# Kernel optimization log

Measured on AMD Instinct MI355X. Metric: run time of the kernel, lower is better.

Reference implementation:

```python
import jax, jax.numpy as jnp
import numpy as np

EMBED, IN_DIM, HID, LAYERS, NVIEW = 1024, 256, 256, 3, 6


def _lstm_layer(x_seq, Wih, Whh, bih, bhh):
    # x_seq: [BM, N, D]; torch LSTM gate order i,f,g,o
    BM = x_seq.shape[0]
    h0 = jnp.zeros((BM, HID), x_seq.dtype)
    c0 = jnp.zeros((BM, HID), x_seq.dtype)

    def step(carry, x_t):
        h, c = carry
        gates = x_t @ Wih.T + bih + h @ Whh.T + bhh  # [BM, 4H]
        i, f, g, o = jnp.split(gates, 4, axis=-1)
        c = jax.nn.sigmoid(f) * c + jax.nn.sigmoid(i) * jnp.tanh(g)
        h = jax.nn.sigmoid(o) * jnp.tanh(c)
        return (h, c), h

    _, ys = jax.lax.scan(step, (h0, c0), jnp.swapaxes(x_seq, 0, 1))
    return jnp.swapaxes(ys, 0, 1)  # [BM, N, H]


def setup_inputs() -> dict:
    key = jax.random.key(0)
    ks = jax.random.split(key, 16)
    B, M = 32, 256
    s = lambda fan: 1.0 / np.sqrt(fan)
    inp = {
        "b_x_swin": jax.random.normal(ks[0], (B, M, NVIEW, EMBED), jnp.float32),
        "b_x_conv": jax.random.normal(ks[1], (B, M, NVIEW, EMBED), jnp.float32),
        "Wc": jax.random.uniform(ks[2], (EMBED, EMBED), jnp.float32, -s(EMBED), s(EMBED)),
        "bc": jax.random.uniform(ks[3], (EMBED,), jnp.float32, -s(EMBED), s(EMBED)),
        "Win": jax.random.uniform(ks[4], (IN_DIM, EMBED), jnp.float32, -s(EMBED), s(EMBED)),
        "b_in": jax.random.uniform(ks[5], (IN_DIM,), jnp.float32, -s(EMBED), s(EMBED)),
        "Wih": jax.random.uniform(ks[6], (LAYERS, 4 * HID, IN_DIM), jnp.float32, -s(HID), s(HID)),
        "Whh": jax.random.uniform(ks[7], (LAYERS, 4 * HID, HID), jnp.float32, -s(HID), s(HID)),
        "bih": jax.random.uniform(ks[8], (LAYERS, 4 * HID), jnp.float32, -s(HID), s(HID)),
        "bhh": jax.random.uniform(ks[9], (LAYERS, 4 * HID), jnp.float32, -s(HID), s(HID)),
        "Wv": jax.random.uniform(ks[10], (1, HID), jnp.float32, -s(HID), s(HID)),
        "bv": jax.random.uniform(ks[11], (1,), jnp.float32, -s(HID), s(HID)),
        "Ws": jax.random.uniform(ks[12], (1, NVIEW), jnp.float32, -s(NVIEW), s(NVIEW)),
        "bs": jax.random.uniform(ks[13], (1,), jnp.float32, -s(NVIEW), s(NVIEW)),
    }
    return inp


def reference(b_x_swin, b_x_conv, Wc, bc, Win, b_in, Wih, Whh, bih, bhh, Wv, bv, Ws, bs):
    B, M, N, C = b_x_swin.shape
    # fc_conv + exact GELU + residual (vectorized over all samples; same math as per-sample loop)
    x = b_x_swin + jax.nn.gelu(b_x_conv @ Wc.T + bc, approximate=False)
    x = x @ Win.T + b_in                         # [B, M, N, IN_DIM]
    x = x.reshape(B * M, N, IN_DIM)              # LSTM batch = B*M, seq = N
    for l in range(LAYERS):
        x = _lstm_layer(x, Wih[l], Whh[l], bih[l], bhh[l])
    v = (x @ Wv.T + bv).reshape(B, M, N)         # fc_viewport + flatten(1)
    score = (v @ Ws.T + bs).squeeze(-1)          # fc_score -> [B, M]
    return jnp.mean(score, axis=1)               # torch.mean per sample -> [B]
```

## Files before the change

### kernel.cpp

```cpp
#include <hip/hip_runtime.h>
#include <math.h>
#include <stdint.h>

typedef unsigned short u16;
typedef float f32x4 __attribute__((ext_vector_type(4)));
typedef short bf16x8 __attribute__((ext_vector_type(8)));

#define NVIEW 6

__device__ __forceinline__ u16 f2bf(float f){
  unsigned u = __float_as_uint(f);
  u += 0x7FFFu + ((u >> 16) & 1u);
  return (u16)(u >> 16);
}
__device__ __forceinline__ float bf2f(u16 h){
  return __uint_as_float(((unsigned)h) << 16);
}
__device__ __forceinline__ float fsig(float x){
  x = fminf(fmaxf(x, -30.f), 30.f);
  return 1.0f / (1.0f + __expf(-x));
}
__device__ __forceinline__ float ftanh(float x){
  x = fminf(fmaxf(x, -15.f), 15.f);
  float e = __expf(2.0f * x);
  return (e - 1.0f) / (e + 1.0f);
}
__device__ __forceinline__ float gelu_exact(float v){
  float x  = v * 0.70710678118654752f;
  float ax = fabsf(x);
  float t  = 1.0f / fmaf(0.3275911f, ax, 1.0f);
  float p  = t * fmaf(t, fmaf(t, fmaf(t, fmaf(t, 1.061405429f, -1.453152027f),
                                      1.421413741f), -0.284496736f), 0.254829592f);
  float er = copysignf(1.0f - p * __expf(-ax * ax), x);
  return 0.5f * v * (1.0f + er);
}
__device__ __forceinline__ void gload16(const u16* g, u16* l){
  __builtin_amdgcn_global_load_lds((const __attribute__((address_space(1))) unsigned int*)g,
                                   (__attribute__((address_space(3))) unsigned int*)l,
                                   16, 0, 0);
}

__global__ void k_cvt(const float* __restrict__ in, u16* __restrict__ out, long n4){
  long i = (long)blockIdx.x * blockDim.x + threadIdx.x;
  long stride = (long)gridDim.x * blockDim.x;
  for (; i < n4; i += stride){
    const float4 v = ((const float4*)in)[i];
    ushort4 o;
    o.x = f2bf(v.x); o.y = f2bf(v.y); o.z = f2bf(v.z); o.w = f2bf(v.w);
    ((ushort4*)out)[i] = o;
  }
}

__global__ void k_build_wl(const float* __restrict__ Wih, const float* __restrict__ Whh,
                           u16* __restrict__ Wl){
  int idx = blockIdx.x * 256 + threadIdx.x;
  int l   = idx >> 19;
  int rem = idx & 524287;
  int ro  = rem >> 9;
  int k   = rem & 511;
  int u = ro >> 2, q = ro & 3;
  int ri = q * 256 + u;
  float v = (k < 256) ? Wih[(l * 1024 + ri) * 256 + k]
                      : Whh[(l * 1024 + ri) * 256 + (k - 256)];
  Wl[idx] = f2bf(v);
}

__global__ void k_build_bias(const float* __restrict__ bih, const float* __restrict__ bhh,
                             float* __restrict__ biasL, u16* __restrict__ zbuf){
  int idx = blockIdx.x * 256 + threadIdx.x;
  if (idx < 3072){
    int l = idx >> 10; int ro = idx & 1023;
    int u = ro >> 2, q = ro & 3;
    int ri = q * 256 + u;
    biasL[idx] = bih[l * 1024 + ri] + bhh[l * 1024 + ri];
  }
  if (idx < 256) zbuf[idx] = 0;
}

template<int EPI>
__global__ __launch_bounds__(256, 2)
void gemm_dr(const u16* __restrict__ A0, long sA0,
             const u16* __restrict__ A1, long sA1, int K0,
             const u16* __restrict__ Bm, long sB,
             int N, int K, int NBn,
             const float* __restrict__ bias,
             const float* __restrict__ resid,
             u16* __restrict__ outb,
             float* __restrict__ cbuf,
             int tstep)
{
  __shared__ __align__(16) u16 lA[5 * 4096];
  __shared__ __align__(16) u16 lB[5 * 4096];

  const int tid  = threadIdx.x;
  const int lane = tid & 63;
  const int wid  = tid >> 6;
  const int wm = wid >> 1, wn = wid & 1;
  const int l15 = lane & 15, lk = lane >> 4;

  const int nwg = gridDim.x;
  const int qx  = nwg >> 3;
  const int bb  = blockIdx.x;
  const int swz = (bb & 7) * qx + (bb >> 3);
  const long m0 = (long)(swz / NBn) * 128;
  const int  n0 = (swz % NBn) * 128;
  const int  NT = K >> 5;

  const int rA0 = tid >> 2;
  const int cA  = tid & 3;
  const int slog = (((rA0 & 1) << 2) | cA) ^ ((rA0 >> 1) & 7);
  const int srow = (rA0 & ~1) | (slog >> 2);
  const int scol = (slog & 3) << 3;
  const int ldst = rA0 * 32 + cA * 8;

  auto STAGE = [&](int slot, int t){
    const int kb = t << 5;
    const int so = slot * 4096;
    #pragma unroll
    for (int c = 0; c < 2; ++c){
      const int r  = c * 64 + srow;
      const int gc = kb + scol;
      const u16* s = (gc < K0) ? (A0 + (m0 + r) * sA0 + gc)
                               : (A1 + (m0 + r) * sA1 + (gc - K0));
      gload16(s, &lA[so + c * 2048 + ldst]);
    }
    #pragma unroll
    for (int c = 0; c < 2; ++c){
      const int r  = c * 64 + srow;
      const int gc = kb + scol;
      gload16(Bm + (long)(n0 + r) * sB + gc, &lB[so + c * 2048 + ldst]);
    }
  };

  f32x4 acc[4][4];
  #pragma unroll
  for (int i = 0; i < 4; ++i)
    #pragma unroll
    for (int j = 0; j < 4; ++j)
      acc[i][j] = (f32x4){0.f, 0.f, 0.f, 0.f};

  const int spA = (((l15 & 1) << 2) | lk) ^ (l15 >> 1);
  const int rdA = (wm * 32 + (l15 >> 1)) * 64 + spA * 8;
  const int rdB = (wn * 32 + (l15 >> 1)) * 64 + spA * 8;

  auto COMPUTE = [&](int slot){
    const int so = slot * 4096;
    bf16x8 af[4], bq[4];
    #pragma unroll
    for (int mf = 0; mf < 4; ++mf)
      af[mf] = *(const bf16x8*)&lA[so + rdA + mf * 512];
    #pragma unroll
    for (int nf = 0; nf < 4; ++nf)
      bq[nf] = *(const bf16x8*)&lB[so + rdB + nf * 512];
    #pragma unroll
    for (int mf = 0; mf < 4; ++mf)
      #pragma unroll
      for (int nf = 0; nf < 4; ++nf)
        acc[mf][nf] = __builtin_amdgcn_mfma_f32_16x16x32_bf16(af[mf], bq[nf], acc[mf][nf], 0, 0, 0);
  };

  STAGE(0, 0); STAGE(1, 1); STAGE(2, 2); STAGE(3, 3);

  int sr = 0, sw = 4;
  for (int t = 0; t + 4 <= NT; ++t){
    asm volatile("s_waitcnt vmcnt(12)" ::: "memory");
    asm volatile("s_barrier" ::: "memory");
    if (t + 4 < NT){ STAGE(sw, t + 4); }
    COMPUTE(sr);
    sr = (sr == 4) ? 0 : sr + 1;
    sw = (sw == 4) ? 0 : sw + 1;
  }
  asm volatile("s_waitcnt vmcnt(8)" ::: "memory");
  asm volatile("s_barrier" ::: "memory");
  COMPUTE(sr); sr = (sr == 4) ? 0 : sr + 1;
  asm volatile("s_waitcnt vmcnt(4)" ::: "memory");
  asm volatile("s_barrier" ::: "memory");
  COMPUTE(sr); sr = (sr == 4) ? 0 : sr + 1;
  asm volatile("s_waitcnt vmcnt(0)" ::: "memory");
  asm volatile("s_barrier" ::: "memory");
  COMPUTE(sr);

  if (EPI == 0 || EPI == 1){
    #pragma unroll
    for (int mf = 0; mf < 4; ++mf){
      #pragma unroll
      for (int nf = 0; nf < 4; ++nf){
        int  n    = n0 + wn * 64 + nf * 16 + l15;
        long mrow = m0 + wm * 64 + mf * 16 + lk * 4;
        float bz = bias[n];
        #pragma unroll
        for (int r = 0; r < 4; ++r){
          float v = acc[mf][nf][r] + bz;
          long off = (mrow + r) * N + n;
          if (EPI == 0) v = gelu_exact(v) + resid[off];
          outb[off] = f2bf(v);
        }
      }
    }
  } else {
    const int a  = lane & 3;
    const int qb = lane & ~3;
    #pragma unroll
    for (int mf = 0; mf < 4; ++mf){
      #pragma unroll
      for (int nf = 0; nf < 4; ++nf){
        int n = n0 + wn * 64 + nf * 16 + l15;
        float bz = bias[n];
        float v0 = acc[mf][nf][0] + bz;
        float v1 = acc[mf][nf][1] + bz;
        float v2 = acc[mf][nf][2] + bz;
        float v3 = acc[mf][nf][3] + bz;
        float s0 = (a == 0) ? v0 : (a == 1) ? v1 : (a == 2) ? v2 : v3;
        float s1 = (a == 0) ? v1 : (a == 1) ? v2 : (a == 2) ? v3 : v0;
        float s2 = (a == 0) ? v2 : (a == 1) ? v3 : (a == 2) ? v0 : v1;
        float s3 = (a == 0) ? v3 : (a == 1) ? v0 : (a == 2) ? v1 : v2;
        float r0 = s0;
        float r1 = __shfl(s1, qb + ((a + 3) & 3));
        float r2 = __shfl(s2, qb + ((a + 2) & 3));
        float r3 = __shfl(s3, qb + ((a + 1) & 3));
        float wi = (a == 0) ? r0 : (a == 1) ? r1 : (a == 2) ? r2 : r3;
        float wf = (a == 1) ? r0 : (a == 2) ? r1 : (a == 3) ? r2 : r3;
        float wg = (a == 2) ? r0 : (a == 3) ? r1 : (a == 0) ? r2 : r3;
        float wo = (a == 3) ? r0 : (a == 0) ? r1 : (a == 1) ? r2 : r3;
        long row = m0 + wm * 64 + mf * 16 + lk * 4 + a;
        int  u   = ((n0 + wn * 64 + nf * 16) >> 2) + (l15 >> 2);
        float c_old = (tstep == 0) ? 0.0f : cbuf[row * 256 + u];
        float ii = fsig(wi), ff = fsig(wf), gg = ftanh(wg), oo = fsig(wo);
        float cn = ff * c_old + ii * gg;
        float hn = oo * ftanh(cn);
        cbuf[row * 256 + u] = cn;
        outb[(row * NVIEW + tstep) * 256 + u] = f2bf(hn);
      }
    }
  }
}

__global__ void k_score(const u16* __restrict__ X3, const float* __restrict__ Wv,
                        const float* __restrict__ bv, const float* __restrict__ Ws,
                        const float* __restrict__ bs, float* __restrict__ score){
  int lane = threadIdx.x & 63;
  int bm = blockIdx.x * 4 + (threadIdx.x >> 6);
  const u16* row = X3 + (long)bm * (NVIEW * 256);
  float4 wv = *(const float4*)(Wv + lane * 4);
  float p = 0.f;
  #pragma unroll
  for (int n = 0; n < NVIEW; ++n){
    ushort4 xv = *(const ushort4*)(row + n * 256 + lane * 4);
    float d = bf2f(xv.x) * wv.x + bf2f(xv.y) * wv.y + bf2f(xv.z) * wv.z + bf2f(xv.w) * wv.w;
    p += Ws[n] * d;
  }
  #pragma unroll
  for (int off = 32; off; off >>= 1) p += __shfl_xor(p, off);
  if (lane == 0){
    float sw = Ws[0] + Ws[1] + Ws[2] + Ws[3] + Ws[4] + Ws[5];
    score[bm] = p + bv[0] * sw + bs[0];
  }
}

__global__ void k_mean(const float* __restrict__ score, float* __restrict__ out){
  __shared__ float red[256];
  int b = blockIdx.x, tid = threadIdx.x;
  red[tid] = score[b * 256 + tid];
  __syncthreads();
  for (int s = 128; s > 0; s >>= 1){
    if (tid < s) red[tid] += red[tid + s];
    __syncthreads();
  }
  if (tid == 0) out[b] = red[0] * (1.0f / 256.0f);
}

extern "C" void kernel_launch(void* const* d_in, const int* in_sizes, int n_in,
                              void* d_out, int out_size, void* d_ws, size_t ws_size,
                              hipStream_t stream){
  const float* swin = (const float*)d_in[0];
  const float* conv = (const float*)d_in[1];
  const float* Wc   = (const float*)d_in[2];
  const float* bc   = (const float*)d_in[3];
  const float* Win  = (const float*)d_in[4];
  const float* b_in = (const float*)d_in[5];
  const float* Wih  = (const float*)d_in[6];
  const float* Whh  = (const float*)d_in[7];
  const float* bih  = (const float*)d_in[8];
  const float* bhh  = (const float*)d_in[9];
  const float* Wv   = (const float*)d_in[10];
  const float* bv   = (const float*)d_in[11];
  const float* Ws   = (const float*)d_in[12];
  const float* bs   = (const float*)d_in[13];
  float* out = (float*)d_out;

  char* w = (char*)d_ws;
  u16*  convb = (u16*)(w);
  u16*  X0    = (u16*)(w);
  u16*  XA    = (u16*)(w + 25165824);
  u16*  XB    = (u16*)(w + 50331648);
  float* cbuf = (float*)(w + 75497472);
  u16*  Y     = (u16*)(w + 100663296);
  u16*  Wcb   = (u16*)(w + 201326592);
  u16*  Winb  = (u16*)(w + 203423744);
  u16*  Wl    = (u16*)(w + 203948032);
  float* biasL= (float*)(w + 207093760);
  u16*  zbuf  = (u16*)(w + 207106048);
  float* scoreb = (float*)(w + 207106560);

  k_cvt<<<4096, 256, 0, stream>>>(conv, convb, 49152L * 1024 / 4);
  k_cvt<<<512, 256, 0, stream>>>(Wc, Wcb, 1048576 / 4);
  k_cvt<<<128, 256, 0, stream>>>(Win, Winb, 262144 / 4);
  k_build_wl<<<6144, 256, 0, stream>>>(Wih, Whh, Wl);
  k_build_bias<<<12, 256, 0, stream>>>(bih, bhh, biasL, zbuf);

  gemm_dr<0><<<3072, 256, 0, stream>>>(
      convb, 1024L, convb, 1024L, 1024,
      Wcb, 1024L, 1024, 1024, 8, bc, swin, Y, (float*)nullptr, 0);

  gemm_dr<1><<<768, 256, 0, stream>>>(
      Y, 1024L, Y, 1024L, 1024,
      Winb, 1024L, 256, 1024, 2, b_in, (const float*)nullptr, X0, (float*)nullptr, 0);

  const u16* xin = X0;
  u16* xout = XA;
  for (int l = 0; l < 3; ++l){
    for (int t = 0; t < 6; ++t){
      const u16* a1 = (t == 0) ? zbuf : (xout + (t - 1) * 256);
      long s1 = (t == 0) ? 0L : 1536L;
      gemm_dr<2><<<512, 256, 0, stream>>>(
          xin + t * 256, 1536L, a1, s1, 256,
          Wl + l * 1024 * 512, 512L, 1024, 512, 8,
          biasL + l * 1024, (const float*)nullptr,
          xout, cbuf, t);
    }
    if (l == 0){ xin = XA; xout = XB; }
    else if (l == 1){ xin = XB; xout = XA; }
  }

  k_score<<<2048, 256, 0, stream>>>(XA, Wv, bv, Ws, bs, scoreb);
  k_mean<<<32, 256, 0, stream>>>(scoreb, out);
}
```

Before: 739.1 us.

## Replace fc_conv GEMM with 256x256-tile 8-wave ping-pong pipelined kernel

Adds a new gemm8 kernel that computes the large fc_conv GEMM (49152x1024x1024) with 256x256 output tiles over 512-thread blocks. It uses double-buffered swizzled LDS, inline ds_read_b128 with immediate offsets, explicit waitcnt and barrier phasing, and setprio around the MFMA bursts. The larger tile is meant to raise data reuse per block and overlap global loads with MFMA work, cutting memory traffic and LDS stalls. In exchange it uses 128KB of LDS, heavy register pressure and hand-scheduled synchronization. It also assumes K is a multiple of 128.

```diff
diff --git a/kernel.cpp b/kernel.cpp
--- a/kernel.cpp
+++ b/kernel.cpp
@@ -75,6 +75,141 @@
     biasL[idx] = bih[l * 1024 + ri] + bhh[l * 1024 + ri];
   }
   if (idx < 256) zbuf[idx] = 0;
+}
+
+#define DSRI(dst, addr, imm) \
+  asm volatile("ds_read_b128 %0, %1 offset:%2" : "=v"(dst) : "v"(addr), "i"(imm))
+
+template<int EPI>
+__global__ __launch_bounds__(512, 2)
+void gemm8(const u16* __restrict__ A, long sA,
+           const u16* __restrict__ Bm, long sB,
+           int N, int K, int NBn,
+           const float* __restrict__ bias,
+           const float* __restrict__ resid,
+           u16* __restrict__ outb)
+{
+  __shared__ __align__(128) u16 sh[65536];
+
+  const int tid  = threadIdx.x;
+  const int lane = tid & 63;
+  const int wv   = tid >> 6;
+  const int wm   = wv >> 2;
+  const int wn   = wv & 3;
+  const int l15  = lane & 15, lk = lane >> 4;
+  const int w2   = wv * 2;
+
+  const int nwg = gridDim.x;
+  const int qx  = nwg >> 3;
+  const int bb  = blockIdx.x;
+  const int swz = (bb & 7) * qx + (bb >> 3);
+  const long m0 = (long)(swz / NBn) * 256;
+  const int  n0 = (swz % NBn) * 256;
+  const int  NT  = K >> 6;
+  const int  NIT = NT >> 1;
+
+  const u16* aSrc = A  + (m0 + (lane >> 3)) * sA + (((lane & 7) ^ (lane >> 3)) << 3);
+  const u16* bSrc = Bm + ((long)n0 + (lane >> 3)) * sB + (((lane & 7) ^ (lane >> 3)) << 3);
+
+  auto STA8 = [&](int buf, int half, int t){
+    const u16* s = aSrc + ((long)(half * 128 + w2 * 8)) * sA + ((long)t << 6);
+    u16* d = &sh[buf * 16384 + half * 8192 + w2 * 512 + lane * 8];
+    gload16(s, d);
+    gload16(s + 8 * sA, d + 512);
+  };
+  auto STB8 = [&](int buf, int half, int t){
+    const u16* s = bSrc + ((long)(half * 128 + w2 * 8)) * sB + ((long)t << 6);
+    u16* d = &sh[32768 + buf * 16384 + half * 8192 + w2 * 512 + lane * 8];
+    gload16(s, d);
+    gload16(s + 8 * sB, d + 512);
+  };
+
+  const unsigned ldsBase = (unsigned)(uintptr_t)&sh[0];
+  const unsigned spb = (unsigned)((lk ^ (l15 & 7)) << 4);
+  const unsigned aRd0 = ldsBase + wm * 16384 + l15 * 128 + spb;
+  const unsigned aRd1 = aRd0 ^ 64;
+  const unsigned bRd0 = ldsBase + 65536 + (wn >> 1) * 16384 + ((wn & 1) * 64 + l15) * 128 + spb;
+  const unsigned bRd1 = bRd0 ^ 64;
+
+#define RDA(BUF, G, KS, DST) do{ const unsigned _a = (KS) ? aRd1 : aRd0;          \
+    DSRI(DST[0], _a, (BUF)*32768 + (G)*8192 + 0);                                 \
+    DSRI(DST[1], _a, (BUF)*32768 + (G)*8192 + 2048);                              \
+    DSRI(DST[2], _a, (BUF)*32768 + (G)*8192 + 4096);                              \
+    DSRI(DST[3], _a, (BUF)*32768 + (G)*8192 + 6144); }while(0)
+#define RDB(BUF, KS, DST) do{ const unsigned _b = (KS) ? bRd1 : bRd0;             \
+    DSRI(DST[0], _b, (BUF)*32768 + 0);                                            \
+    DSRI(DST[1], _b, (BUF)*32768 + 2048);                                         \
+    DSRI(DST[2], _b, (BUF)*32768 + 4096);                                         \
+    DSRI(DST[3], _b, (BUF)*32768 + 6144); }while(0)
+
+  f32x4 acc[8][4];
+  #pragma unroll
+  for (int i = 0; i < 8; ++i)
+    #pragma unroll
+    for (int j = 0; j < 4; ++j)
+      acc[i][j] = (f32x4){0.f, 0.f, 0.f, 0.f};
+
+  bf16x8 aF0[4], aF1[4], bF0[4], bF1[4];
+
+  STA8(0, 0, 0); STA8(0, 1, 0); STB8(0, 0, 0); STB8(0, 1, 0);
+  STB8(1, 0, 1); STB8(1, 1, 1);
+  asm volatile("s_waitcnt vmcnt(4)" ::: "memory");
+  __builtin_amdgcn_s_barrier();
+  RDA(0, 0, 0, aF0); RDB(0, 0, bF0);
+
+#define PH(G, AU, BU, RDS, STG, VM) {                                             \
+    RDS;                                                                          \
+    STG;                                                                          \
+    __builtin_amdgcn_s_barrier();                                                 \
+    asm volatile("s_waitcnt lgkmcnt(0)" ::: "memory");                            \
+    __builtin_amdgcn_sched_barrier(0);                                            \
+    __builtin_amdgcn_s_setprio(1);                                                \
+    _Pragma("unroll") for (int i = 0; i < 4; ++i)                                 \
+      _Pragma("unroll") for (int nf = 0; nf < 4; ++nf)                            \
+        acc[(G)*4 + i][nf] = __builtin_amdgcn_mfma_f32_16x16x32_bf16(             \
+            AU[i], BU[nf], acc[(G)*4 + i][nf], 0, 0, 0);                          \
+    __builtin_amdgcn_s_setprio(0);                                                \
+    VM;                                                                           \
+    __builtin_amdgcn_s_barrier(); }
+
+#define VM2C { if (nl) { asm volatile("s_waitcnt vmcnt(2)" ::: "memory"); }        \
+               else    { asm volatile("s_waitcnt vmcnt(0)" ::: "memory"); } }
+#define NOVM { }
+
+  for (int I = 0; I < NIT; ++I){
+    const int t1 = 2 * I + 1;
+    const bool nl = (I < NIT - 1);
+    PH(0, aF0, bF0, RDA(0,1,0,aF1),                 STA8(1,0,t1),               NOVM)
+    PH(1, aF1, bF0, { RDA(0,0,1,aF0); RDB(0,1,bF1);}, STA8(1,1,t1),             NOVM)
+    PH(0, aF0, bF1, RDA(0,1,1,aF1),                 if (nl) STB8(0,0,t1+1);,    VM2C)
+    PH(1, aF1, bF1, { RDA(1,0,0,aF0); RDB(1,0,bF0);}, if (nl) STB8(0,1,t1+1);, NOVM)
+    PH(0, aF0, bF0, RDA(1,1,0,aF1),                 if (nl) STA8(0,0,t1+1);,    NOVM)
+    PH(1, aF1, bF0, { RDA(1,0,1,aF0); RDB(1,1,bF1);}, if (nl) STA8(0,1,t1+1);, NOVM)
+    PH(0, aF0, bF1, RDA(1,1,1,aF1),                 if (nl) STB8(1,0,t1+2);,    VM2C)
+    PH(1, aF1, bF1, { RDA(0,0,0,aF0); RDB(0,0,bF0);}, if (nl) STB8(1,1,t1+2);, NOVM)
+  }
+#undef PH
+#undef VM2C
+#undef NOVM
+#undef RDA
+#undef RDB
+
+  #pragma unroll
+  for (int mf = 0; mf < 8; ++mf){
+    #pragma unroll
+    for (int nf = 0; nf < 4; ++nf){
+      const int n = n0 + wn * 64 + nf * 16 + l15;
+      const float bz = bias[n];
+      const long mrow = m0 + wm * 128 + mf * 16 + lk * 4;
+      #pragma unroll
+      for (int r = 0; r < 4; ++r){
+        float v = acc[mf][nf][r] + bz;
+        const long off = (mrow + r) * (long)N + n;
+        if (EPI == 0) v = gelu_exact(v) + resid[off];
+        outb[off] = f2bf(v);
+      }
+    }
+  }
 }
 
 template<int EPI>
@@ -308,9 +443,8 @@
   k_build_wl<<<6144, 256, 0, stream>>>(Wih, Whh, Wl);
   k_build_bias<<<12, 256, 0, stream>>>(bih, bhh, biasL, zbuf);
 
-  gemm_dr<0><<<3072, 256, 0, stream>>>(
-      convb, 1024L, convb, 1024L, 1024,
-      Wcb, 1024L, 1024, 1024, 8, bc, swin, Y, (float*)nullptr, 0);
+  gemm8<0><<<768, 512, 0, stream>>>(convb, 1024L, Wcb, 1024L,
+                                    1024, 1024, 4, bc, swin, Y);
 
   gemm_dr<1><<<768, 256, 0, stream>>>(
       Y, 1024L, Y, 1024L, 1024,
```

After: 812.7 us. 1.1x slower.

## Fuse all LSTM layers and timesteps into one persistent kernel

Applied to the files above, without the earlier changes.

Replaces the 18 per-timestep GEMM launches with a single k_lstm kernel. Each block owns 32 sequences across all 3 layers and 6 steps, keeping the cell state in registers and h in LDS, and streams the weights through a 3-slot LDS ring. This removes the launch overhead, the cbuf global round trips and the re-reading of h from global memory. In exchange only 256 blocks at occupancy 1 run, and every block re-streams the full weight set from L2 at each step.

```diff
diff --git a/kernel.cpp b/kernel.cpp
--- a/kernel.cpp
+++ b/kernel.cpp
@@ -66,7 +66,7 @@
 }
 
 __global__ void k_build_bias(const float* __restrict__ bih, const float* __restrict__ bhh,
-                             float* __restrict__ biasL, u16* __restrict__ zbuf){
+                             float* __restrict__ biasL){
   int idx = blockIdx.x * 256 + threadIdx.x;
   if (idx < 3072){
     int l = idx >> 10; int ro = idx & 1023;
@@ -74,20 +74,16 @@
     int ri = q * 256 + u;
     biasL[idx] = bih[l * 1024 + ri] + bhh[l * 1024 + ri];
   }
-  if (idx < 256) zbuf[idx] = 0;
 }
 
 template<int EPI>
 __global__ __launch_bounds__(256, 2)
 void gemm_dr(const u16* __restrict__ A0, long sA0,
-             const u16* __restrict__ A1, long sA1, int K0,
              const u16* __restrict__ Bm, long sB,
              int N, int K, int NBn,
              const float* __restrict__ bias,
              const float* __restrict__ resid,
-             u16* __restrict__ outb,
-             float* __restrict__ cbuf,
-             int tstep)
+             u16* __restrict__ outb)
 {
   __shared__ __align__(16) u16 lA[5 * 4096];
   __shared__ __align__(16) u16 lB[5 * 4096];
@@ -119,16 +115,12 @@
     #pragma unroll
     for (int c = 0; c < 2; ++c){
       const int r  = c * 64 + srow;
-      const int gc = kb + scol;
-      const u16* s = (gc < K0) ? (A0 + (m0 + r) * sA0 + gc)
-                               : (A1 + (m0 + r) * sA1 + (gc - K0));
-      gload16(s, &lA[so + c * 2048 + ldst]);
+      gload16(A0 + (m0 + r) * sA0 + (kb + scol), &lA[so + c * 2048 + ldst]);
     }
     #pragma unroll
     for (int c = 0; c < 2; ++c){
       const int r  = c * 64 + srow;
-      const int gc = kb + scol;
-      gload16(Bm + (long)(n0 + r) * sB + gc, &lB[so + c * 2048 + ldst]);
+      gload16(Bm + (long)(n0 + r) * sB + (kb + scol), &lB[so + c * 2048 + ldst]);
     }
   };
 
@@ -180,56 +172,170 @@
   asm volatile("s_barrier" ::: "memory");
   COMPUTE(sr);
 
-  if (EPI == 0 || EPI == 1){
-    #pragma unroll
-    for (int mf = 0; mf < 4; ++mf){
-      #pragma unroll
-      for (int nf = 0; nf < 4; ++nf){
-        int  n    = n0 + wn * 64 + nf * 16 + l15;
-        long mrow = m0 + wm * 64 + mf * 16 + lk * 4;
-        float bz = bias[n];
+  #pragma unroll
+  for (int mf = 0; mf < 4; ++mf){
+    #pragma unroll
+    for (int nf = 0; nf < 4; ++nf){
+      int  n    = n0 + wn * 64 + nf * 16 + l15;
+      long mrow = m0 + wm * 64 + mf * 16 + lk * 4;
+      float bz = bias[n];
+      #pragma unroll
+      for (int r = 0; r < 4; ++r){
+        float v = acc[mf][nf][r] + bz;
+        long off = (mrow + r) * N + n;
+        if (EPI == 0) v = gelu_exact(v) + resid[off];
+        outb[off] = f2bf(v);
+      }
+    }
+  }
+}
+
+__global__ __launch_bounds__(256, 1)
+void k_lstm(const u16* __restrict__ X0, const u16* __restrict__ Wl,
+            const float* __restrict__ biasL,
+            u16* __restrict__ HA, u16* __restrict__ HB)
+{
+  __shared__ __align__(16) u16 lA[16384];
+  __shared__ __align__(16) u16 lB[3 * 16384];
+
+  const int tid  = threadIdx.x;
+  const int lane = tid & 63;
+  const int wv   = tid >> 6;
+  const int l15  = lane & 15, lk = lane >> 4;
+  const int ax   = l15 & 7;
+  const int spB  = (((l15 & 1) << 2) | lk) ^ (l15 >> 1);
+  const int a    = lane & 3;
+  const int qb   = lane & ~3;
+  const long R   = (long)blockIdx.x * 32;
+
+  const int rB0 = tid >> 2;
+  const int cB  = tid & 3;
+  const int slogB = (((rB0 & 1) << 2) | cB) ^ ((rB0 >> 1) & 7);
+  const int srowB = (rB0 & ~1) | (slogB >> 2);
+  const int scolB = (slogB & 3) << 3;
+  const int ldstB = rB0 * 32 + cB * 8;
+
+  auto STB = [&](int g){
+    if (g < 576){
+      const int lw  = g / 192;
+      const int hcl = g % 32;
+      const int ring = g % 3;
+      const u16* src = Wl + (long)lw * 524288 + (long)(hcl & 1) * 262144 + (hcl >> 1) * 32;
+      u16* dst = &lB[ring * 16384];
+      #pragma unroll
+      for (int ch = 0; ch < 8; ++ch)
+        gload16(src + (long)(ch * 64 + srowB) * 512 + scolB, dst + ch * 2048 + ldstB);
+    }
+  };
+
+  const int xr_ = tid >> 3;
+  const int xcb = tid & 7;
+  const int xk  = xr_ & 7;
+
+  f32x4 acc[2][2][8];
+  float cc[2][2][8];
+  float bv[2][8];
+
+  int g = 0;
+  STB(0); STB(1);
+
+  for (int l = 0; l < 3; ++l){
+    const u16* xsrc = (l == 0) ? X0 : ((l == 1) ? HA : HB);
+    u16* hdst = (l == 1) ? HB : HA;
+    #pragma unroll
+    for (int hf = 0; hf < 2; ++hf)
+      #pragma unroll
+      for (int nt = 0; nt < 8; ++nt){
+        bv[hf][nt] = biasL[l * 1024 + hf * 512 + wv * 128 + nt * 16 + l15];
         #pragma unroll
-        for (int r = 0; r < 4; ++r){
-          float v = acc[mf][nf][r] + bz;
-          long off = (mrow + r) * N + n;
-          if (EPI == 0) v = gelu_exact(v) + resid[off];
-          outb[off] = f2bf(v);
-        }
+        for (int mt = 0; mt < 2; ++mt) cc[mt][hf][nt] = 0.f;
       }
-    }
-  } else {
-    const int a  = lane & 3;
-    const int qb = lane & ~3;
-    #pragma unroll
-    for (int mf = 0; mf < 4; ++mf){
-      #pragma unroll
-      for (int nf = 0; nf < 4; ++nf){
-        int n = n0 + wn * 64 + nf * 16 + l15;
-        float bz = bias[n];
-        float v0 = acc[mf][nf][0] + bz;
-        float v1 = acc[mf][nf][1] + bz;
-        float v2 = acc[mf][nf][2] + bz;
-        float v3 = acc[mf][nf][3] + bz;
-        float s0 = (a == 0) ? v0 : (a == 1) ? v1 : (a == 2) ? v2 : v3;
-        float s1 = (a == 0) ? v1 : (a == 1) ? v2 : (a == 2) ? v3 : v0;
-        float s2 = (a == 0) ? v2 : (a == 1) ? v3 : (a == 2) ? v0 : v1;
-        float s3 = (a == 0) ? v3 : (a == 1) ? v0 : (a == 2) ? v1 : v2;
-        float r0 = s0;
-        float r1 = __shfl(s1, qb + ((a + 3) & 3));
-        float r2 = __shfl(s2, qb + ((a + 2) & 3));
-        float r3 = __shfl(s3, qb + ((a + 1) & 3));
-        float wi = (a == 0) ? r0 : (a == 1) ? r1 : (a == 2) ? r2 : r3;
-        float wf = (a == 1) ? r0 : (a == 2) ? r1 : (a == 3) ? r2 : r3;
-        float wg = (a == 2) ? r0 : (a == 3) ? r1 : (a == 0) ? r2 : r3;
-        float wo = (a == 3) ? r0 : (a == 0) ? r1 : (a == 1) ? r2 : r3;
-        long row = m0 + wm * 64 + mf * 16 + lk * 4 + a;
-        int  u   = ((n0 + wn * 64 + nf * 16) >> 2) + (l15 >> 2);
-        float c_old = (tstep == 0) ? 0.0f : cbuf[row * 256 + u];
-        float ii = fsig(wi), ff = fsig(wf), gg = ftanh(wg), oo = fsig(wo);
-        float cn = ff * c_old + ii * gg;
-        float hn = oo * ftanh(cn);
-        cbuf[row * 256 + u] = cn;
-        outb[(row * NVIEW + tstep) * 256 + u] = f2bf(hn);
+    __syncthreads();
+    {
+      bf16x8 z = (bf16x8){0,0,0,0,0,0,0,0};
+      #pragma unroll
+      for (int j = 0; j < 4; ++j)
+        *(bf16x8*)&lA[xr_ * 512 + (32 + ((4 * xcb + j) ^ xk)) * 8] = z;
+    }
+    for (int t = 0; t < 6; ++t){
+      bf16x8 xv[4];
+      const u16* xp = xsrc + ((R + xr_) * 6 + t) * 256 + xcb * 32;
+      #pragma unroll
+      for (int j = 0; j < 4; ++j) xv[j] = *(const bf16x8*)(xp + j * 8);
+      __syncthreads();
+      #pragma unroll
+      for (int mt = 0; mt < 2; ++mt)
+        #pragma unroll
+        for (int hf = 0; hf < 2; ++hf)
+          #pragma unroll
+          for (int nt = 0; nt < 8; ++nt)
+            acc[mt][hf][nt] = (f32x4){0.f, 0.f, 0.f, 0.f};
+      #pragma unroll
+      for (int j = 0; j < 4; ++j)
+        *(bf16x8*)&lA[xr_ * 512 + ((4 * xcb + j) ^ xk) * 8] = xv[j];
+      asm volatile("s_waitcnt lgkmcnt(0)" ::: "memory");
+      __builtin_amdgcn_s_barrier();
+
+#define HALF(HF)                                                               \
+      {                                                                        \
+        asm volatile("s_waitcnt vmcnt(8)" ::: "memory");                       \
+        asm volatile("s_barrier" ::: "memory");                                \
+        STB(g + 2);                                                            \
+        const int ring = g % 3;                                                \
+        bf16x8 af[2], bq[8];                                                   \
+        _Pragma("unroll") for (int mt = 0; mt < 2; ++mt)                       \
+          af[mt] = *(const bf16x8*)&lA[(mt * 16 + l15) * 512 +                 \
+                                       ((ktc * 4 + lk) ^ ax) * 8];             \
+        _Pragma("unroll") for (int nt = 0; nt < 8; ++nt)                       \
+          bq[nt] = *(const bf16x8*)&lB[ring * 16384 +                          \
+                     (wv * 64 + nt * 8 + (l15 >> 1)) * 64 + spB * 8];          \
+        _Pragma("unroll") for (int mt = 0; mt < 2; ++mt)                       \
+          _Pragma("unroll") for (int nt = 0; nt < 8; ++nt)                     \
+            acc[mt][HF][nt] = __builtin_amdgcn_mfma_f32_16x16x32_bf16(         \
+                af[mt], bq[nt], acc[mt][HF][nt], 0, 0, 0);                     \
+        ++g;                                                                   \
+      }
+      for (int ktc = 0; ktc < 16; ++ktc){ HALF(0) HALF(1) }
+#undef HALF
+
+      #pragma unroll
+      for (int mt = 0; mt < 2; ++mt)
+        #pragma unroll
+        for (int hf = 0; hf < 2; ++hf)
+          #pragma unroll
+          for (int nt = 0; nt < 8; ++nt){
+            const float bz = bv[hf][nt];
+            float v0 = acc[mt][hf][nt][0] + bz;
+            float v1 = acc[mt][hf][nt][1] + bz;
+            float v2 = acc[mt][hf][nt][2] + bz;
+            float v3 = acc[mt][hf][nt][3] + bz;
+            float s0 = (a == 0) ? v0 : (a == 1) ? v1 : (a == 2) ? v2 : v3;
+            float s1 = (a == 0) ? v1 : (a == 1) ? v2 : (a == 2) ? v3 : v0;
+            float s2 = (a == 0) ? v2 : (a == 1) ? v3 : (a == 2) ? v0 : v1;
+            float s3 = (a == 0) ? v3 : (a == 1) ? v0 : (a == 2) ? v1 : v2;
+            float r0 = s0;
+            float r1 = __shfl(s1, qb + ((a + 3) & 3));
+            float r2 = __shfl(s2, qb + ((a + 2) & 3));
+            float r3 = __shfl(s3, qb + ((a + 1) & 3));
+            float wi = (a == 0) ? r0 : (a == 1) ? r1 : (a == 2) ? r2 : r3;
+            float wf = (a == 1) ? r0 : (a == 2) ? r1 : (a == 3) ? r2 : r3;
+            float wg = (a == 2) ? r0 : (a == 3) ? r1 : (a == 0) ? r2 : r3;
+            float wo = (a == 3) ? r0 : (a == 0) ? r1 : (a == 1) ? r2 : r3;
+            const int rloc = mt * 16 + lk * 4 + a;
+            const int u    = hf * 128 + wv * 32 + nt * 4 + (l15 >> 2);
+            float co = cc[mt][hf][nt];
+            float ii = fsig(wi), ff = fsig(wf), gg = ftanh(wg), oo = fsig(wo);
+            float cn = ff * co + ii * gg;
+            float hn = oo * ftanh(cn);
+            cc[mt][hf][nt] = cn;
+            lA[rloc * 512 + (32 + ((u >> 3) ^ (rloc & 7))) * 8 + (u & 7)] = f2bf(hn);
+          }
+      asm volatile("s_waitcnt lgkmcnt(0)" ::: "memory");
+      __builtin_amdgcn_s_barrier();
+      #pragma unroll
+      for (int j = 0; j < 4; ++j){
+        bf16x8 hv = *(const bf16x8*)&lA[xr_ * 512 + (32 + ((4 * xcb + j) ^ xk)) * 8];
+        *(bf16x8*)(hdst + ((R + xr_) * 6 + t) * 256 + xcb * 32 + j * 8) = hv;
       }
     }
   }
@@ -293,44 +399,26 @@
   u16*  X0    = (u16*)(w);
   u16*  XA    = (u16*)(w + 25165824);
   u16*  XB    = (u16*)(w + 50331648);
-  float* cbuf = (float*)(w + 75497472);
   u16*  Y     = (u16*)(w + 100663296);
   u16*  Wcb   = (u16*)(w + 201326592);
   u16*  Winb  = (u16*)(w + 203423744);
   u16*  Wl    = (u16*)(w + 203948032);
   float* biasL= (float*)(w + 207093760);
-  u16*  zbuf  = (u16*)(w + 207106048);
   float* scoreb = (float*)(w + 207106560);
 
   k_cvt<<<4096, 256, 0, stream>>>(conv, convb, 49152L * 1024 / 4);
   k_cvt<<<512, 256, 0, stream>>>(Wc, Wcb, 1048576 / 4);
   k_cvt<<<128, 256, 0, stream>>>(Win, Winb, 262144 / 4);
   k_build_wl<<<6144, 256, 0, stream>>>(Wih, Whh, Wl);
-  k_build_bias<<<12, 256, 0, stream>>>(bih, bhh, biasL, zbuf);
+  k_build_bias<<<12, 256, 0, stream>>>(bih, bhh, biasL);
 
   gemm_dr<0><<<3072, 256, 0, stream>>>(
-      convb, 1024L, convb, 1024L, 1024,
-      Wcb, 1024L, 1024, 1024, 8, bc, swin, Y, (float*)nullptr, 0);
+      convb, 1024L, Wcb, 1024L, 1024, 1024, 8, bc, swin, Y);
 
   gemm_dr<1><<<768, 256, 0, stream>>>(
-      Y, 1024L, Y, 1024L, 1024,
-      Winb, 1024L, 256, 1024, 2, b_in, (const float*)nullptr, X0, (float*)nullptr, 0);
-
-  const u16* xin = X0;
-  u16* xout = XA;
-  for (int l = 0; l < 3; ++l){
-    for (int t = 0; t < 6; ++t){
-      const u16* a1 = (t == 0) ? zbuf : (xout + (t - 1) * 256);
-      long s1 = (t == 0) ? 0L : 1536L;
-      gemm_dr<2><<<512, 256, 0, stream>>>(
-          xin + t * 256, 1536L, a1, s1, 256,
-          Wl + l * 1024 * 512, 512L, 1024, 512, 8,
-          biasL + l * 1024, (const float*)nullptr,
-          xout, cbuf, t);
-    }
-    if (l == 0){ xin = XA; xout = XB; }
-    else if (l == 1){ xin = XB; xout = XA; }
-  }
+      Y, 1024L, Winb, 1024L, 256, 1024, 2, b_in, (const float*)nullptr, X0);
+
+  k_lstm<<<256, 256, 0, stream>>>(X0, Wl, biasL, XA, XB);
 
   k_score<<<2048, 256, 0, stream>>>(XA, Wv, bv, Ws, bs, scoreb);
   k_mean<<<32, 256, 0, stream>>>(scoreb, out);
```

New measurement: 951.5 us, median of 2. 28.7% more time.
